# Performance work log

Measured on AMD Instinct MI355X. Metric: run time of the kernel, lower is better.

## Reference

```python
import jax, jax.numpy as jnp
import numpy as np

B, C, N, K = 4, 128, 4096, 16
COUT = 128
GROUPS = 4


def _gather(x, idx):
    # x: [B, C, N, 1], idx: [B, N, K] -> [B, C, N, K]
    x2 = x[..., 0]  # [B, C, N]
    return jax.vmap(lambda xb, ib: xb[:, ib])(x2, idx)


def setup_inputs() -> dict:
    key = jax.random.key(0)
    k1, k2, k3, k4 = jax.random.split(key, 4)
    x = jax.random.normal(k1, (B, C, N, 1), dtype=jnp.float32)
    edge_index = jax.random.randint(k2, (2, B, N, K), 0, N, dtype=jnp.int64)
    fan_in = 2 * C // GROUPS  # kaiming_normal fan_in for 1x1 grouped conv
    weight = jax.random.normal(k3, (COUT, 2 * C // GROUPS, 1, 1), dtype=jnp.float32) * np.sqrt(2.0 / fan_in)
    bias = jnp.zeros((COUT,), dtype=jnp.float32)
    return {"x": x, "edge_index": edge_index, "weight": weight, "bias": bias}


def reference(x, edge_index, weight, bias):
    x_i = _gather(x, edge_index[1])          # [B, C, N, K]
    x_j = _gather(x, edge_index[0])          # [B, C, N, K]
    feat = jnp.concatenate([x_i, x_j - x_i], axis=1)  # [B, 2C, N, K]
    # grouped 1x1 conv, groups=4
    cin_g = 2 * C // GROUPS
    cout_g = COUT // GROUPS
    fg = feat.reshape(B, GROUPS, cin_g, N, K)
    wg = weight[..., 0, 0].reshape(GROUPS, cout_g, cin_g)
    out = jnp.einsum('bgcnk,goc->bgonk', fg, wg).reshape(B, COUT, N, K)
    out = out + bias[None, :, None, None]
    out = jax.nn.relu(out)
    return jnp.mean(out, axis=-1, keepdims=True)  # [B, COUT, N, 1]
```

## Files before the change

kernel.cpp:

```cpp
#include <hip/hip_runtime.h>


#define BB   4
#define CC   128
#define NN   4096
#define KK   16
#define CO   128

__global__ __launch_bounds__(512) void precompute_y(
    const float* __restrict__ x,
    const float* __restrict__ w,
    float* __restrict__ Y)
{
    const int lane = threadIdx.x & 63;
    const int wv = __builtin_amdgcn_readfirstlane((int)(threadIdx.x >> 6));

    const int bid  = blockIdx.x;
    const int work = (bid & 7) * ((int)gridDim.x >> 3) + (bid >> 3);

    const int gnode = work * 64 + lane;
    const int b = gnode >> 12;
    const int n = gnode & (NN - 1);

    const int obase = wv * 16;
    const int cbase = ((wv >> 1) & 1) * 64;

    const float* xp = x + ((size_t)(b * CC + cbase)) * NN + n;
    float xr[64];
#pragma unroll
    for (int c = 0; c < 64; ++c) xr[c] = xp[(size_t)c * NN];

    const float* wp = w + obase * 64;
    float buf[16];
#pragma unroll
    for (int oi = 0; oi < 16; ++oi) {
        float acc = 0.f;
#pragma unroll
        for (int c = 0; c < 64; ++c) acc = fmaf(wp[oi * 64 + c], xr[c], acc);
        buf[oi] = acc;
    }

    float* yp = Y + (size_t)gnode * CO + obase;
#pragma unroll
    for (int q = 0; q < 4; ++q) {
        float4 v = make_float4(buf[4*q], buf[4*q+1], buf[4*q+2], buf[4*q+3]);
        *(float4*)(yp + 4 * q) = v;
    }
}

#define NPB 16
__global__ __launch_bounds__(256) void edge_gather(
    const int*   __restrict__ ei,
    const float* __restrict__ Y,
    const float* __restrict__ bias,
    float* __restrict__ out)
{
    __shared__ float tile[NPB][129];

    const int lane = threadIdx.x & 63;
    const int wv   = threadIdx.x >> 6;

    const int bid  = blockIdx.x;
    const int work = (bid & 7) * ((int)gridDim.x >> 3) + (bid >> 3);

    const int node0 = work * NPB;
    const int b     = node0 >> 12;
    const float* Yb = Y + (size_t)b * NN * CO;

    const float blo = bias[lane];
    const float bhi = bias[lane + 64];

    const int* i0p = ei;
    const int* i1p = ei + (size_t)BB * NN * KK;

    for (int t = wv; t < NPB; t += 4) {
        const int gnode = node0 + t;
        const size_t ib = (size_t)gnode * KK;
        const int v0 = i0p[ib + (lane & 15)];
        const int v1 = i1p[ib + (lane & 15)];

        float acc0 = 0.f, acc1 = 0.f;
#pragma unroll
        for (int k = 0; k < KK; ++k) {
            const int i1 = __shfl(v1, k);
            const int j  = __shfl(v0, k);
            const float* Yi = Yb + (size_t)i1 * CO;
            const float* Yj = Yb + (size_t)j  * CO;
            const float a  = Yi[lane];
            const float c1 = Yi[lane + 64];
            const float c2 = Yj[lane + 64];
            acc0 += fmaxf(a + blo, 0.f);
            acc1 += fmaxf(c2 - c1 + bhi, 0.f);
        }
        tile[t][lane]      = acc0 * (1.f / KK);
        tile[t][lane + 64] = acc1 * (1.f / KK);
    }
    __syncthreads();

    const int n0   = node0 & (NN - 1);
    const int nloc = lane & 15;
    const int ob   = wv * 32 + (lane >> 4) * 8;
#pragma unroll
    for (int r = 0; r < 8; ++r) {
        const int o = ob + r;
        out[((size_t)(b * CO + o)) * NN + n0 + nloc] = tile[nloc][o];
    }
}

__global__ __launch_bounds__(128) void edgeconv_fallback(
    const int*   __restrict__ ei,
    const float* __restrict__ x,
    const float* __restrict__ w,
    const float* __restrict__ bias,
    float* __restrict__ out)
{
    const int bn = blockIdx.x;
    const int b  = bn >> 12;
    const int n  = bn & (NN - 1);
    const int o  = threadIdx.x;
    const int g  = o >> 5;
    const int cbase = (g & 1) * 64;
    const bool useJ = (g >= 2);

    const float* xb = x + (size_t)b * CC * NN;
    const int* i0p = ei;
    const int* i1p = ei + (size_t)BB * NN * KK;

    float wr[64];
#pragma unroll
    for (int c = 0; c < 64; ++c) wr[c] = w[o * 64 + c];

    float acc = 0.f;
    for (int k = 0; k < KK; ++k) {
        const int i1 = i1p[(size_t)bn * KK + k];
        const int j  = i0p[(size_t)bn * KK + k];
        float dot = 0.f;
#pragma unroll
        for (int c = 0; c < 64; ++c) {
            const float xi = xb[(size_t)(cbase + c) * NN + i1];
            const float f  = useJ ? (xb[(size_t)(cbase + c) * NN + j] - xi) : xi;
            dot = fmaf(wr[c], f, dot);
        }
        acc += fmaxf(dot + bias[o], 0.f);
    }
    out[((size_t)(b * CO + o)) * NN + n] = acc * (1.f / KK);
}

extern "C" void kernel_launch(void* const* d_in, const int* in_sizes, int n_in,
                              void* d_out, int out_size, void* d_ws, size_t ws_size,
                              hipStream_t stream) {
    const float* x    = (const float*)d_in[0];
    const int*   ei   = (const int*)d_in[1];
    const float* w    = (const float*)d_in[2];
    const float* bias = (const float*)d_in[3];
    float* out = (float*)d_out;

    const size_t need = (size_t)BB * NN * CO * sizeof(float);
    if (ws_size >= need) {
        float* Y = (float*)d_ws;
        precompute_y<<<dim3(BB * NN / 64), dim3(512), 0, stream>>>(x, w, Y);
        edge_gather<<<dim3(BB * NN / NPB), dim3(256), 0, stream>>>(ei, Y, bias, out);
    } else {
        edgeconv_fallback<<<dim3(BB * NN), dim3(128), 0, stream>>>(ei, x, w, bias, out);
    }
}
```

Measured before the change: 96.87 us.

## Vectorize edge gather with float2 loads and 512-thread blocks

Restructures the edge_gather kernel so each lane loads a float2 of the precomputed Y row: the low half-wave handles the x_i channels and the high half-wave loads both i and j rows for the difference channels. This avoids the redundant third scalar load per neighbor. Block size doubles to 512 with two nodes per wave, indices are made wave-uniform with readfirstlane, and the transpose writeout uses float4 LDS reads. The k loop is only partially unrolled (4), which may reduce memory-level parallelism compared with the full unroll.

```diff
diff --git a/kernel.cpp b/kernel.cpp
--- a/kernel.cpp
+++ b/kernel.cpp
@@ -49,13 +49,13 @@
 }
 
 #define NPB 16
-__global__ __launch_bounds__(256) void edge_gather(
+__global__ __launch_bounds__(512, 8) void edge_gather(
     const int*   __restrict__ ei,
     const float* __restrict__ Y,
     const float* __restrict__ bias,
     float* __restrict__ out)
 {
-    __shared__ float tile[NPB][129];
+    __shared__ float tile[NPB][132];
 
     const int lane = threadIdx.x & 63;
     const int wv   = threadIdx.x >> 6;
@@ -67,44 +67,47 @@
     const int b     = node0 >> 12;
     const float* Yb = Y + (size_t)b * NN * CO;
 
-    const float blo = bias[lane];
-    const float bhi = bias[lane + 64];
+    const float2 b2 = *(const float2*)(bias + 2 * lane);
+    const bool hi = (lane >= 32);
 
     const int* i0p = ei;
     const int* i1p = ei + (size_t)BB * NN * KK;
 
-    for (int t = wv; t < NPB; t += 4) {
+#pragma unroll
+    for (int s = 0; s < 2; ++s) {
+        const int t = wv + 8 * s;
         const int gnode = node0 + t;
         const size_t ib = (size_t)gnode * KK;
         const int v0 = i0p[ib + (lane & 15)];
         const int v1 = i1p[ib + (lane & 15)];
 
-        float acc0 = 0.f, acc1 = 0.f;
-#pragma unroll
+        float accx = 0.f, accy = 0.f;
+#pragma unroll 4
         for (int k = 0; k < KK; ++k) {
-            const int i1 = __shfl(v1, k);
-            const int j  = __shfl(v0, k);
-            const float* Yi = Yb + (size_t)i1 * CO;
-            const float* Yj = Yb + (size_t)j  * CO;
-            const float a  = Yi[lane];
-            const float c1 = Yi[lane + 64];
-            const float c2 = Yj[lane + 64];
-            acc0 += fmaxf(a + blo, 0.f);
-            acc1 += fmaxf(c2 - c1 + bhi, 0.f);
+            const int i1 = __builtin_amdgcn_readfirstlane(__shfl(v1, k));
+            const int j  = __builtin_amdgcn_readfirstlane(__shfl(v0, k));
+            const float2 yi = *(const float2*)(Yb + (size_t)i1 * CO + 2 * lane);
+            float2 yj = make_float2(0.f, 0.f);
+            if (hi) yj = *(const float2*)(Yb + (size_t)j * CO + 2 * lane);
+            const float vx = hi ? (yj.x - yi.x) : yi.x;
+            const float vy = hi ? (yj.y - yi.y) : yi.y;
+            accx += fmaxf(vx + b2.x, 0.f);
+            accy += fmaxf(vy + b2.y, 0.f);
         }
-        tile[t][lane]      = acc0 * (1.f / KK);
-        tile[t][lane + 64] = acc1 * (1.f / KK);
+        *(float2*)&tile[t][2 * lane] =
+            make_float2(accx * (1.f / KK), accy * (1.f / KK));
     }
     __syncthreads();
 
     const int n0   = node0 & (NN - 1);
     const int nloc = lane & 15;
-    const int ob   = wv * 32 + (lane >> 4) * 8;
-#pragma unroll
-    for (int r = 0; r < 8; ++r) {
-        const int o = ob + r;
-        out[((size_t)(b * CO + o)) * NN + n0 + nloc] = tile[nloc][o];
-    }
+    const int ob   = wv * 16 + (lane >> 4) * 4;
+    const float4 v = *(const float4*)&tile[nloc][ob];
+    float* op = out + ((size_t)(b * CO + ob)) * NN + n0 + nloc;
+    op[0]              = v.x;
+    op[(size_t)NN]     = v.y;
+    op[2 * (size_t)NN] = v.z;
+    op[3 * (size_t)NN] = v.w;
 }
 
 __global__ __launch_bounds__(128) void edgeconv_fallback(
@@ -159,7 +162,7 @@
     if (ws_size >= need) {
         float* Y = (float*)d_ws;
         precompute_y<<<dim3(BB * NN / 64), dim3(512), 0, stream>>>(x, w, Y);
-        edge_gather<<<dim3(BB * NN / NPB), dim3(256), 0, stream>>>(ei, Y, bias, out);
+        edge_gather<<<dim3(BB * NN / NPB), dim3(512), 0, stream>>>(ei, Y, bias, out);
     } else {
         edgeconv_fallback<<<dim3(BB * NN), dim3(128), 0, stream>>>(ei, x, w, bias, out);
     }
```

Result: slower. 104.1 us (+7.5%).
